# Optimization experiments

Measured on AMD Instinct MI355X. Metric: run time of the kernel, lower is better.

## Reference

```python
import jax, jax.numpy as jnp
import numpy as np

MAX_DEG = 10
MIN_DEG = 0
N_FEAT = 128
NB_FILTER = 128
BATCH = 128
DEG_COUNT = 30000                      # atoms per degree bucket (static)
N_ATOMS = (MAX_DEG + 1) * DEG_COUNT    # 330000, atoms sorted by degree (deg0 first)
NB_AFFINE = 3 * MAX_DEG + (2 - MIN_DEG)  # 32
EPS = 1e-5


def setup_inputs() -> dict:
    key = jax.random.key(0)
    ks = jax.random.split(key, 16)
    atoms = jax.random.normal(ks[0], (N_ATOMS, N_FEAT), dtype=jnp.float32)
    membership = jax.random.randint(ks[1], (N_ATOMS,), 0, BATCH)
    # deg_slice[d] = [start, count] for degree d (atoms sorted by degree)
    deg_slice = jnp.stack([jnp.arange(MAX_DEG + 1) * DEG_COUNT,
                           jnp.full((MAX_DEG + 1,), DEG_COUNT)], axis=1)
    inp = {"atoms": atoms, "deg_slice": deg_slice, "membership": membership}
    for d in range(1, MAX_DEG + 1):
        inp[f"adj{d}"] = jax.random.randint(ks[1 + d], (DEG_COUNT, d), 0, N_ATOMS)
    glorot = (2.0 / (N_FEAT + NB_FILTER)) ** 0.5
    inp["W"] = jax.random.normal(ks[12], (NB_AFFINE, N_FEAT, NB_FILTER), dtype=jnp.float32) * glorot
    inp["b"] = jnp.zeros((NB_AFFINE, NB_FILTER), dtype=jnp.float32)
    inp["gamma"] = jnp.ones((NB_FILTER,), dtype=jnp.float32)
    inp["beta"] = jnp.zeros((NB_FILTER,), dtype=jnp.float32)
    return inp


def _self_slice(atoms, deg):
    return jax.lax.dynamic_slice_in_dim(atoms, deg * DEG_COUNT, DEG_COUNT, axis=0)


def _norm(x, gamma, beta):
    m = jnp.mean(x, axis=-1, keepdims=True)
    std = jnp.sqrt(jnp.var(x, axis=-1, keepdims=True) + EPS)
    return gamma * ((x - m) / (std + EPS)) + beta


def _forward(atoms, W, b, gamma, beta, membership, adjs):
    # W consumption order matches the TF iterator: for deg=1..max_deg -> (rel, self),
    # then deg0 self at index 2*MAX_DEG, then gather affines deg1..max_deg, deg0 last.
    rel_outs = [None] * (MAX_DEG + 1)
    gather_outs = [None] * (MAX_DEG + 1)
    for d in range(1, MAX_DEG + 1):
        neigh = jnp.sum(atoms[adjs[d - 1]], axis=1)          # (COUNT, F) gather+sum
        self_a = _self_slice(atoms, d)                        # (COUNT, F)
        i_rel, i_self = 2 * (d - 1), 2 * d - 1
        rel_outs[d] = (neigh @ W[i_rel] + b[i_rel]) + (self_a @ W[i_self] + b[i_self])
        i_g = 2 * MAX_DEG + d
        gather_outs[d] = self_a @ W[i_g] + b[i_g]
    self0 = _self_slice(atoms, 0)
    rel_outs[0] = self0 @ W[2 * MAX_DEG] + b[2 * MAX_DEG]
    gather_outs[0] = self0 @ W[NB_AFFINE - 1] + b[NB_AFFINE - 1]

    activated = jnp.concatenate(rel_outs, axis=0)             # (N_ATOMS, NB_FILTER)
    gathered = jnp.concatenate(gather_outs, axis=0)           # (N_ATOMS, NB_FILTER)
    # graph_gather: per-molecule sum (dynamic_partition + reduce_sum)
    atom_gather = jax.ops.segment_sum(gathered, membership, num_segments=BATCH)

    xn = _norm(activated, gamma, beta)                        # per-row "BN" as in source
    yn = _norm(atom_gather, gamma, beta)
    # gather_node: per-molecule max of normalized atom features
    g = jax.ops.segment_max(xn, membership, num_segments=BATCH)
    return xn, yn, g


def reference(atoms, deg_slice, membership, adj1, adj2, adj3, adj4, adj5,
              adj6, adj7, adj8, adj9, adj10, W, b, gamma, beta):
    adjs = (adj1, adj2, adj3, adj4, adj5, adj6, adj7, adj8, adj9, adj10)
    return _forward(atoms, W, b, gamma, beta, membership, adjs)
```

## Files before the change

kernel.cpp:

```cpp
#include <hip/hip_runtime.h>
#include <stdint.h>

#define MAX_DEG   10
#define DEG_COUNT 30000
#define N_ATOMS   330000
#define NF        128
#define BATCH     128
#define SORT_BLOCKS 256

typedef __attribute__((ext_vector_type(8))) short bf16x8;
typedef __attribute__((ext_vector_type(4))) float f32x4;

__device__ __forceinline__ float bf2f(unsigned short h) {
  union { unsigned u; float f; } v; v.u = ((unsigned)h) << 16; return v.f;
}
__device__ __forceinline__ unsigned short f2bf(float f) {
  union { float f; unsigned u; } v; v.f = f;
  unsigned u = v.u;
  unsigned r = (u + 0x7fffu + ((u >> 16) & 1u)) >> 16;
  return (unsigned short)r;
}

struct AdjPtrs { const int* p[10]; };

#define NEG_INF_BITS 0xFF800000

__global__ __launch_bounds__(256) void k_cast(const float4* __restrict__ src,
                                              ushort4* __restrict__ dst) {
  size_t i = (size_t)blockIdx.x * 256 + threadIdx.x;
  float4 v = src[i];
  ushort4 o;
  o.x = f2bf(v.x); o.y = f2bf(v.y); o.z = f2bf(v.z); o.w = f2bf(v.w);
  dst[i] = o;
}

__global__ __launch_bounds__(256) void k_build_b(const float* __restrict__ W,
                                                 unsigned short* __restrict__ BcatT) {
  int idx = blockIdx.x * 256 + threadIdx.x;
  if (idx >= 11 * 128 * 256) return;
  int d = idx >> 15;
  int rem = idx & 32767;
  int n = rem >> 8;
  int k = rem & 255;
  float v;
  if (k < 128) {
    v = (d >= 1) ? W[(2 * (d - 1)) * 16384 + k * 128 + n] : 0.f;
  } else {
    int ks = k - 128;
    int wi = (d >= 1) ? (2 * d - 1) : 20;
    v = W[wi * 16384 + ks * 128 + n];
  }
  BcatT[idx] = f2bf(v);
}

__global__ __launch_bounds__(256) void k_build_bias(const float* __restrict__ b,
                                                    float* __restrict__ biascat) {
  int idx = blockIdx.x * 256 + threadIdx.x;
  if (idx >= 11 * 128) return;
  int d = idx >> 7, n = idx & 127;
  float f = (d >= 1) ? (b[(2 * (d - 1)) * 128 + n] + b[(2 * d - 1) * 128 + n])
                     : b[20 * 128 + n];
  biascat[idx] = f;
}

template<int D>
__device__ __forceinline__ void nsum_phase0(const unsigned* __restrict__ atomsU,
                                            const int* __restrict__ abase,
                                            unsigned* __restrict__ NS,
                                            int rowTile, int wave, int lane) {
  for (int it = 0; it < 8; ++it) {
    int iloc = wave * 16 + it * 2;
    int r0 = rowTile * 128 + iloc;
    int sw0 = lane ^ ((iloc & 7) << 2);
    int sw1 = lane ^ (((iloc + 1) & 7) << 2);
    if (r0 < DEG_COUNT - 1) {
      const int* a = abase + (size_t)r0 * D;
      int myIdx = (lane < 2 * D) ? a[lane] : 0;
      unsigned xs[2 * D];
#pragma unroll
      for (int j = 0; j < 2 * D; ++j) {
        int nbr = __shfl(myIdx, j, 64);
        xs[j] = atomsU[(size_t)nbr * 64 + lane];
      }
      float s0a = 0.f, s1a = 0.f, s0b = 0.f, s1b = 0.f;
#pragma unroll
      for (int j = 0; j < D; ++j) {
        s0a += bf2f((unsigned short)(xs[j] & 0xffff));
        s1a += bf2f((unsigned short)(xs[j] >> 16));
      }
#pragma unroll
      for (int j = D; j < 2 * D; ++j) {
        s0b += bf2f((unsigned short)(xs[j] & 0xffff));
        s1b += bf2f((unsigned short)(xs[j] >> 16));
      }
      NS[(size_t)iloc * 64 + sw0]       = (unsigned)f2bf(s0a) | ((unsigned)f2bf(s1a) << 16);
      NS[(size_t)(iloc + 1) * 64 + sw1] = (unsigned)f2bf(s0b) | ((unsigned)f2bf(s1b) << 16);
    } else {
      const int* a = abase + (size_t)(DEG_COUNT - 1) * D;
      int myIdx = (lane < D) ? a[lane] : 0;
      unsigned xs[D];
#pragma unroll
      for (int j = 0; j < D; ++j) {
        int nbr = __shfl(myIdx, j, 64);
        xs[j] = atomsU[(size_t)nbr * 64 + lane];
      }
      float s0 = 0.f, s1 = 0.f;
#pragma unroll
      for (int j = 0; j < D; ++j) {
        s0 += bf2f((unsigned short)(xs[j] & 0xffff));
        s1 += bf2f((unsigned short)(xs[j] >> 16));
      }
      unsigned p = (unsigned)f2bf(s0) | ((unsigned)f2bf(s1) << 16);
      NS[(size_t)iloc * 64 + sw0] = p;
      NS[(size_t)(iloc + 1) * 64 + sw1] = p;
    }
  }
}

__global__ __launch_bounds__(512, 4) void k_gemm(
    const unsigned short* __restrict__ atomsBf,
    AdjPtrs adj,
    const unsigned short* __restrict__ BcatT,
    const float* __restrict__ biascat,
    const float* __restrict__ gamma,
    const float* __restrict__ beta,
    float* __restrict__ out0)
{
  const int d = blockIdx.y;
  const int rowTile = blockIdx.x;
  const int tid = threadIdx.x;
  const int lane = tid & 63;
  const int wave = tid >> 6;
  const int m16 = lane & 15;
  const int g = lane >> 4;

  __shared__ unsigned short Bs[128 * 256];
  unsigned* NS = (unsigned*)Bs;

  const unsigned short* Bd = BcatT + d * 32768;
  const unsigned* atomsU = (const unsigned*)atomsBf;

  const int rowBase = rowTile * 128 + wave * 16;
  bf16x8 af[8];
  {
    int rbL = rowBase + m16; if (rbL > DEG_COUNT - 1) rbL = DEG_COUNT - 1;
    size_t gr = (size_t)d * DEG_COUNT + rbL;
#pragma unroll
    for (int ks = 4; ks < 8; ++ks)
      af[ks] = *(const bf16x8*)(atomsBf + gr * 128 + (ks - 4) * 32 + g * 8);
  }

  if (d > 0) {
    const int* abase = adj.p[d - 1];
    switch (d) {
      case 1:  nsum_phase0<1>(atomsU, abase, NS, rowTile, wave, lane); break;
      case 2:  nsum_phase0<2>(atomsU, abase, NS, rowTile, wave, lane); break;
      case 3:  nsum_phase0<3>(atomsU, abase, NS, rowTile, wave, lane); break;
      case 4:  nsum_phase0<4>(atomsU, abase, NS, rowTile, wave, lane); break;
      case 5:  nsum_phase0<5>(atomsU, abase, NS, rowTile, wave, lane); break;
      case 6:  nsum_phase0<6>(atomsU, abase, NS, rowTile, wave, lane); break;
      case 7:  nsum_phase0<7>(atomsU, abase, NS, rowTile, wave, lane); break;
      case 8:  nsum_phase0<8>(atomsU, abase, NS, rowTile, wave, lane); break;
      case 9:  nsum_phase0<9>(atomsU, abase, NS, rowTile, wave, lane); break;
      default: nsum_phase0<10>(atomsU, abase, NS, rowTile, wave, lane); break;
    }
    __syncthreads();
    const char* nsb = (const char*)NS;
    const int rowb = (wave * 16 + m16) * 256;
    const int sw = (m16 & 7) << 4;
#pragma unroll
    for (int ks = 0; ks < 4; ++ks)
      af[ks] = *(const bf16x8*)(nsb + ((rowb + ks * 64 + g * 16) ^ sw));
    __syncthreads();
  } else {
    bf16x8 z = {0, 0, 0, 0, 0, 0, 0, 0};
#pragma unroll
    for (int ks = 0; ks < 4; ++ks) af[ks] = z;
  }

#pragma unroll
  for (int it = 0; it < 8; ++it) {
    int flat = it * 512 + tid;
    int row = flat >> 5;
    int c = flat & 31;
    uint4 v = *(const uint4*)(Bd + row * 256 + c * 8);
    int kb = (c * 16) ^ ((row & 7) << 4);
    *(uint4*)((char*)Bs + row * 512 + kb) = v;
  }

  __syncthreads();

  const int ldsMask = (m16 & 7) << 4;

  f32x4 acc[8];
#pragma unroll
  for (int ct = 0; ct < 8; ++ct) acc[ct] = (f32x4){0.f, 0.f, 0.f, 0.f};

#pragma unroll
  for (int ct = 0; ct < 8; ++ct) {
    const char* bbase = (const char*)Bs + (ct * 16 + m16) * 512;
    bf16x8 bf[8];
#pragma unroll
    for (int ks = 0; ks < 8; ++ks)
      bf[ks] = *(const bf16x8*)(bbase + ((ks * 64 + g * 16) ^ ldsMask));
#pragma unroll
    for (int ks = 0; ks < 8; ++ks)
      acc[ct] = __builtin_amdgcn_mfma_f32_16x16x32_bf16(af[ks], bf[ks], acc[ct], 0, 0, 0);
  }

  float bias_[8], gam[8], bet[8];
#pragma unroll
  for (int ct = 0; ct < 8; ++ct) {
    bias_[ct] = biascat[d * 128 + ct * 16 + m16];
    gam[ct] = gamma[ct * 16 + m16];
    bet[ct] = beta[ct * 16 + m16];
  }

#pragma unroll
  for (int ct = 0; ct < 8; ++ct)
#pragma unroll
    for (int r = 0; r < 4; ++r) acc[ct][r] += bias_[ct];

  float s[4], qq[4];
#pragma unroll
  for (int r = 0; r < 4; ++r) {
    s[r] = 0.f; qq[r] = 0.f;
#pragma unroll
    for (int ct = 0; ct < 8; ++ct) {
      float v = acc[ct][r];
      s[r] += v; qq[r] += v * v;
    }
  }
#pragma unroll
  for (int off = 8; off >= 1; off >>= 1) {
#pragma unroll
    for (int r = 0; r < 4; ++r) {
      s[r]  += __shfl_xor(s[r],  off, 64);
      qq[r] += __shfl_xor(qq[r], off, 64);
    }
  }

#pragma unroll
  for (int r = 0; r < 4; ++r) {
    int rb = rowBase + g * 4 + r;
    float mean = s[r] * (1.0f / 128.0f);
    float var  = qq[r] * (1.0f / 128.0f) - mean * mean;
    float inv  = 1.0f / (sqrtf(var + 1e-5f) + 1e-5f);
    if (rb < DEG_COUNT) {
      size_t grow = (size_t)d * DEG_COUNT + rb;
#pragma unroll
      for (int ct = 0; ct < 8; ++ct)
        out0[grow * 128 + ct * 16 + m16] = gam[ct] * ((acc[ct][r] - mean) * inv) + bet[ct];
    }
  }
}

__global__ __launch_bounds__(256) void k_hist2(const int* __restrict__ membership,
                                               int* __restrict__ blockHist) {
  __shared__ int bins[BATCH];
  int tid = threadIdx.x;
  if (tid < BATCH) bins[tid] = 0;
  __syncthreads();
  const int chunk = (N_ATOMS + SORT_BLOCKS - 1) / SORT_BLOCKS;
  int lo = blockIdx.x * chunk, hi = min(lo + chunk, N_ATOMS);
  for (int i = lo + tid; i < hi; i += 256)
    atomicAdd(&bins[membership[i]], 1);
  __syncthreads();
  if (tid < BATCH) blockHist[blockIdx.x * BATCH + tid] = bins[tid];
}

__global__ __launch_bounds__(128) void k_scan2(const int* __restrict__ blockHist,
                                               int* __restrict__ off,
                                               int* __restrict__ base,
                                               int* __restrict__ hist) {
  int m = threadIdx.x;
  int tot = 0;
  for (int b = 0; b < SORT_BLOCKS; ++b) tot += blockHist[b * BATCH + m];
  hist[m] = tot;
  __shared__ int t[BATCH];
  t[m] = tot;
  __syncthreads();
  int acc = 0;
  for (int i = 0; i < m; ++i) acc += t[i];
  base[m] = acc;
  int run = acc;
  for (int b = 0; b < SORT_BLOCKS; ++b) {
    off[b * BATCH + m] = run;
    run += blockHist[b * BATCH + m];
  }
}

__global__ __launch_bounds__(256) void k_scatter2(const int* __restrict__ membership,
                                                  const int* __restrict__ off,
                                                  int* __restrict__ perm) {
  __shared__ int bins[BATCH];
  int tid = threadIdx.x;
  if (tid < BATCH) bins[tid] = off[blockIdx.x * BATCH + tid];
  __syncthreads();
  const int chunk = (N_ATOMS + SORT_BLOCKS - 1) / SORT_BLOCKS;
  int lo = blockIdx.x * chunk, hi = min(lo + chunk, N_ATOMS);
  for (int i = lo + tid; i < hi; i += 256) {
    int m = membership[i];
    int pos = atomicAdd(&bins[m], 1);
    perm[pos] = i;
  }
}

__global__ __launch_bounds__(512) void k_msum(
    const unsigned* __restrict__ atomsU,
    const int* __restrict__ perm,
    const int* __restrict__ base,
    const int* __restrict__ hist,
    float* __restrict__ Spart,
    int* __restrict__ cntPart)
{
  const int m = blockIdx.x >> 2;
  const int s = blockIdx.x & 3;
  const int b0 = base[m], cnt = hist[m];
  const int lo = b0 + (cnt * s) / 4;
  const int hi = b0 + (cnt * (s + 1)) / 4;
  const int wave = threadIdx.x >> 6, lane = threadIdx.x & 63;

  __shared__ float S[8][11][128];
  __shared__ int C[8][11];
  for (int e = lane; e < 11 * 128; e += 64) S[wave][e >> 7][e & 127] = 0.f;
  if (lane < 11) C[wave][lane] = 0;
  __syncthreads();

  for (int i = lo + wave; i < hi; i += 8) {
    int r = perm[i];
    int d = r / DEG_COUNT;
    unsigned x = atomsU[(size_t)r * 64 + lane];
    S[wave][d][lane]      += bf2f((unsigned short)(x & 0xffff));
    S[wave][d][64 + lane] += bf2f((unsigned short)(x >> 16));
    if (lane == 0) C[wave][d]++;
  }
  __syncthreads();

  for (int e = threadIdx.x; e < 11 * 128; e += 512) {
    int d = e >> 7, p = e & 127;
    float t = 0.f;
#pragma unroll
    for (int w = 0; w < 8; ++w) t += S[w][d][p];
    int col = (p < 64) ? (2 * p) : (2 * (p - 64) + 1);
    Spart[(((size_t)s * 128 + m) * 11 + d) * 128 + col] = t;
  }
  if (threadIdx.x < 11) {
    int t = 0;
#pragma unroll
    for (int w = 0; w < 8; ++w) t += C[w][threadIdx.x];
    cntPart[((size_t)s * 128 + m) * 11 + threadIdx.x] = t;
  }
}

__global__ __launch_bounds__(128) void k_yn(
    const float* __restrict__ Spart,
    const int* __restrict__ cntPart,
    const float* __restrict__ W,
    const float* __restrict__ b,
    const float* __restrict__ gamma,
    const float* __restrict__ beta,
    float* __restrict__ out1)
{
  int m = blockIdx.x;
  int j = threadIdx.x;
  __shared__ float Sm[11][128];
  __shared__ float cw[11];
  for (int e = j; e < 11 * 128; e += 128) {
    int d = e >> 7, c = e & 127;
    float t = 0.f;
#pragma unroll
    for (int sl = 0; sl < 4; ++sl)
      t += Spart[(((size_t)sl * 128 + m) * 11 + d) * 128 + c];
    Sm[d][c] = t;
  }
  if (j < 11) {
    int t = 0;
#pragma unroll
    for (int sl = 0; sl < 4; ++sl) t += cntPart[((size_t)sl * 128 + m) * 11 + j];
    cw[j] = (float)t;
  }
  __syncthreads();

  float acc = 0.f;
  for (int d = 0; d < 11; ++d) {
    int wi = (d >= 1) ? (20 + d) : 31;
    const float* Wd = W + wi * 16384;
    float a0 = 0.f, a1 = 0.f, a2 = 0.f, a3 = 0.f;
    for (int k = 0; k < 128; k += 4) {
      a0 += Sm[d][k]     * Wd[k * 128 + j];
      a1 += Sm[d][k + 1] * Wd[(k + 1) * 128 + j];
      a2 += Sm[d][k + 2] * Wd[(k + 2) * 128 + j];
      a3 += Sm[d][k + 3] * Wd[(k + 3) * 128 + j];
    }
    acc += (a0 + a1) + (a2 + a3);
    acc += cw[d] * b[wi * 128 + j];
  }

  float ws_ = acc, wq = acc * acc;
#pragma unroll
  for (int off = 32; off >= 1; off >>= 1) {
    ws_ += __shfl_xor(ws_, off, 64);
    wq  += __shfl_xor(wq, off, 64);
  }
  __shared__ float red[4];
  int wave = j >> 6, lane = j & 63;
  if (lane == 0) { red[wave * 2] = ws_; red[wave * 2 + 1] = wq; }
  __syncthreads();
  float Ssum = red[0] + red[2], Q = red[1] + red[3];
  float mean = Ssum * (1.f / 128.f);
  float var = Q * (1.f / 128.f) - mean * mean;
  float inv = 1.f / (sqrtf(var + 1e-5f) + 1e-5f);
  out1[m * 128 + j] = gamma[j] * ((acc - mean) * inv) + beta[j];
}

__global__ __launch_bounds__(512) void k_reduce(
    const float2* __restrict__ xnV,
    const int* __restrict__ perm,
    const int* __restrict__ base,
    const int* __restrict__ hist,
    float2* __restrict__ pmax4)
{
  const int m = blockIdx.x >> 2;
  const int s = blockIdx.x & 3;
  const int b0 = base[m], cnt = hist[m];
  const int lo = b0 + (cnt * s) / 4;
  const int hi = b0 + (cnt * (s + 1)) / 4;
  const int wave = threadIdx.x >> 6, lane = threadIdx.x & 63;

  const float NEG_INF = __int_as_float((int)NEG_INF_BITS);
  float mx0 = NEG_INF, mx1 = NEG_INF;

#pragma unroll 4
  for (int i = lo + wave; i < hi; i += 8) {
    int r = perm[i];
    float2 x = xnV[(size_t)r * 64 + lane];
    mx0 = fmaxf(mx0, x.x);
    mx1 = fmaxf(mx1, x.y);
  }

  __shared__ float2 maxT[8][64];
  maxT[wave][lane] = make_float2(mx0, mx1);
  __syncthreads();

  if (threadIdx.x < 64) {
    int l = threadIdx.x;
    float2 mm = maxT[0][l];
#pragma unroll
    for (int w = 1; w < 8; ++w) {
      float2 b = maxT[w][l]; mm.x = fmaxf(mm.x, b.x); mm.y = fmaxf(mm.y, b.y);
    }
    pmax4[(s * 128 + m) * 64 + l] = mm;
  }
}

__global__ __launch_bounds__(128) void k_final(
    const float* __restrict__ pmax4,
    float* __restrict__ out2)
{
  int m = blockIdx.x;
  int j = threadIdx.x;
  float g = __int_as_float((int)NEG_INF_BITS);
#pragma unroll
  for (int sl = 0; sl < 4; ++sl)
    g = fmaxf(g, pmax4[(sl * 128 + m) * 128 + j]);
  out2[m * 128 + j] = g;
}

extern "C" void kernel_launch(void* const* d_in, const int* in_sizes, int n_in,
                              void* d_out, int out_size, void* d_ws, size_t ws_size,
                              hipStream_t stream) {
  const float* atoms = (const float*)d_in[0];
  const int* membership = (const int*)d_in[2];
  AdjPtrs adj;
  for (int i = 0; i < 10; ++i) adj.p[i] = (const int*)d_in[3 + i];
  const float* W     = (const float*)d_in[13];
  const float* b     = (const float*)d_in[14];
  const float* gamma = (const float*)d_in[15];
  const float* beta  = (const float*)d_in[16];

  char* ws = (char*)d_ws;
  size_t off = 0;
  unsigned short* atomsBf = (unsigned short*)(ws + off); off += (size_t)N_ATOMS * 128 * 2;
  unsigned short* BcatT   = (unsigned short*)(ws + off); off += (size_t)11 * 128 * 256 * 2;
  float* biascat          = (float*)(ws + off);          off += (size_t)11 * 128 * 4;
  int* perm               = (int*)(ws + off);            off += (size_t)N_ATOMS * 4;
  int* hist               = (int*)(ws + off);            off += 512;
  int* base_              = (int*)(ws + off);            off += 512;
  int* blockHist          = (int*)(ws + off);            off += (size_t)SORT_BLOCKS * BATCH * 4;
  int* offTab             = (int*)(ws + off);            off += (size_t)SORT_BLOCKS * BATCH * 4;
  float* Spart            = (float*)(ws + off);          off += (size_t)4 * 128 * 11 * 128 * 4;
  int* cntPart            = (int*)(ws + off);            off += (size_t)4 * 128 * 11 * 4;
  float* pmax4            = (float*)(ws + off);          off += (size_t)4 * 128 * 128 * 4;

  float* out0 = (float*)d_out;
  float* out1 = out0 + (size_t)N_ATOMS * 128;
  float* out2 = out1 + 16384;

  hipLaunchKernelGGL(k_cast, dim3(N_ATOMS * 128 / 4 / 256), dim3(256), 0, stream,
                     (const float4*)atoms, (ushort4*)atomsBf);
  hipLaunchKernelGGL(k_build_b, dim3((11 * 128 * 256 + 255) / 256), dim3(256), 0, stream, W, BcatT);
  hipLaunchKernelGGL(k_build_bias, dim3((11 * 128 + 255) / 256), dim3(256), 0, stream, b, biascat);
  hipLaunchKernelGGL(k_hist2, dim3(SORT_BLOCKS), dim3(256), 0, stream, membership, blockHist);
  hipLaunchKernelGGL(k_scan2, dim3(1), dim3(128), 0, stream, blockHist, offTab, base_, hist);
  hipLaunchKernelGGL(k_scatter2, dim3(SORT_BLOCKS), dim3(256), 0, stream, membership, offTab, perm);
  hipLaunchKernelGGL(k_msum, dim3(512), dim3(512), 0, stream,
                     (const unsigned*)atomsBf, perm, base_, hist, Spart, cntPart);
  hipLaunchKernelGGL(k_gemm, dim3(236, 11), dim3(512), 0, stream,
                     atomsBf, adj, BcatT, biascat, gamma, beta, out0);
  hipLaunchKernelGGL(k_reduce, dim3(512), dim3(512), 0, stream,
                     (const float2*)out0, perm, base_, hist, (float2*)pmax4);
  hipLaunchKernelGGL(k_yn, dim3(128), dim3(128), 0, stream,
                     Spart, cntPart, W, b, gamma, beta, out1);
  hipLaunchKernelGGL(k_final, dim3(128), dim3(128), 0, stream, pmax4, out2);
}
```

Baseline: 554.5 us.

## Fuse molecule sum and max reductions into one pass, add nontemporal memory ops

Merges the per-molecule bf16 atom sum (k_msum) and the per-molecule max over normalized outputs (k_reduce) into a single kernel that walks the permutation once and reads both arrays per row. It also folds k_final into k_yn, which removes two launches. The cast kernel's loads, the GEMM epilogue's output stores and the fused reduction's loads are now nontemporal, to limit cache pollution on streaming traffic. The trade-off is that the molecule-sum work now runs after the GEMM instead of before it, and the fused loop carries two gather streams per iteration. The `#pragma unroll 4` that k_reduce had on this loop is dropped.

```diff
diff --git a/kernel.cpp b/kernel.cpp
--- a/kernel.cpp
+++ b/kernel.cpp
@@ -10,6 +10,7 @@
 
 typedef __attribute__((ext_vector_type(8))) short bf16x8;
 typedef __attribute__((ext_vector_type(4))) float f32x4;
+typedef __attribute__((ext_vector_type(2))) float f32x2;
 
 __device__ __forceinline__ float bf2f(unsigned short h) {
   union { unsigned u; float f; } v; v.u = ((unsigned)h) << 16; return v.f;
@@ -25,12 +26,12 @@
 
 #define NEG_INF_BITS 0xFF800000
 
-__global__ __launch_bounds__(256) void k_cast(const float4* __restrict__ src,
+__global__ __launch_bounds__(256) void k_cast(const f32x4* __restrict__ src,
                                               ushort4* __restrict__ dst) {
   size_t i = (size_t)blockIdx.x * 256 + threadIdx.x;
-  float4 v = src[i];
+  f32x4 v = __builtin_nontemporal_load(src + i);
   ushort4 o;
-  o.x = f2bf(v.x); o.y = f2bf(v.y); o.z = f2bf(v.z); o.w = f2bf(v.w);
+  o.x = f2bf(v[0]); o.y = f2bf(v[1]); o.z = f2bf(v[2]); o.w = f2bf(v[3]);
   dst[i] = o;
 }
 
@@ -249,8 +250,10 @@
     if (rb < DEG_COUNT) {
       size_t grow = (size_t)d * DEG_COUNT + rb;
 #pragma unroll
-      for (int ct = 0; ct < 8; ++ct)
-        out0[grow * 128 + ct * 16 + m16] = gam[ct] * ((acc[ct][r] - mean) * inv) + bet[ct];
+      for (int ct = 0; ct < 8; ++ct) {
+        float v = gam[ct] * ((acc[ct][r] - mean) * inv) + bet[ct];
+        __builtin_nontemporal_store(v, out0 + grow * 128 + ct * 16 + m16);
+      }
     }
   }
 }
@@ -306,13 +309,15 @@
   }
 }
 
-__global__ __launch_bounds__(512) void k_msum(
+__global__ __launch_bounds__(512) void k_mreduce(
+    const f32x2* __restrict__ xnV,
     const unsigned* __restrict__ atomsU,
     const int* __restrict__ perm,
     const int* __restrict__ base,
     const int* __restrict__ hist,
     float* __restrict__ Spart,
-    int* __restrict__ cntPart)
+    int* __restrict__ cntPart,
+    float2* __restrict__ pmax4)
 {
   const int m = blockIdx.x >> 2;
   const int s = blockIdx.x & 3;
@@ -323,20 +328,37 @@
 
   __shared__ float S[8][11][128];
   __shared__ int C[8][11];
+  __shared__ float2 maxT[8][64];
   for (int e = lane; e < 11 * 128; e += 64) S[wave][e >> 7][e & 127] = 0.f;
   if (lane < 11) C[wave][lane] = 0;
   __syncthreads();
+
+  const float NEG_INF = __int_as_float((int)NEG_INF_BITS);
+  float mx0 = NEG_INF, mx1 = NEG_INF;
 
   for (int i = lo + wave; i < hi; i += 8) {
     int r = perm[i];
     int d = r / DEG_COUNT;
-    unsigned x = atomsU[(size_t)r * 64 + lane];
-    S[wave][d][lane]      += bf2f((unsigned short)(x & 0xffff));
-    S[wave][d][64 + lane] += bf2f((unsigned short)(x >> 16));
+    f32x2 x = __builtin_nontemporal_load(xnV + (size_t)r * 64 + lane);
+    unsigned a = __builtin_nontemporal_load(atomsU + (size_t)r * 64 + lane);
+    mx0 = fmaxf(mx0, x[0]);
+    mx1 = fmaxf(mx1, x[1]);
+    S[wave][d][lane]      += bf2f((unsigned short)(a & 0xffff));
+    S[wave][d][64 + lane] += bf2f((unsigned short)(a >> 16));
     if (lane == 0) C[wave][d]++;
   }
-  __syncthreads();
-
+  maxT[wave][lane] = make_float2(mx0, mx1);
+  __syncthreads();
+
+  if (threadIdx.x < 64) {
+    int l = threadIdx.x;
+    float2 mm = maxT[0][l];
+#pragma unroll
+    for (int w = 1; w < 8; ++w) {
+      float2 b = maxT[w][l]; mm.x = fmaxf(mm.x, b.x); mm.y = fmaxf(mm.y, b.y);
+    }
+    pmax4[(s * 128 + m) * 64 + l] = mm;
+  }
   for (int e = threadIdx.x; e < 11 * 128; e += 512) {
     int d = e >> 7, p = e & 127;
     float t = 0.f;
@@ -353,17 +375,26 @@
   }
 }
 
-__global__ __launch_bounds__(128) void k_yn(
+__global__ __launch_bounds__(128) void k_ynfinal(
     const float* __restrict__ Spart,
     const int* __restrict__ cntPart,
     const float* __restrict__ W,
     const float* __restrict__ b,
     const float* __restrict__ gamma,
     const float* __restrict__ beta,
-    float* __restrict__ out1)
+    const float* __restrict__ pmax4,
+    float* __restrict__ out1,
+    float* __restrict__ out2)
 {
   int m = blockIdx.x;
   int j = threadIdx.x;
+
+  float g = __int_as_float((int)NEG_INF_BITS);
+#pragma unroll
+  for (int sl = 0; sl < 4; ++sl)
+    g = fmaxf(g, pmax4[(sl * 128 + m) * 128 + j]);
+  out2[m * 128 + j] = g;
+
   __shared__ float Sm[11][128];
   __shared__ float cw[11];
   for (int e = j; e < 11 * 128; e += 128) {
@@ -412,59 +443,6 @@
   float var = Q * (1.f / 128.f) - mean * mean;
   float inv = 1.f / (sqrtf(var + 1e-5f) + 1e-5f);
   out1[m * 128 + j] = gamma[j] * ((acc - mean) * inv) + beta[j];
-}
-
-__global__ __launch_bounds__(512) void k_reduce(
-    const float2* __restrict__ xnV,
-    const int* __restrict__ perm,
-    const int* __restrict__ base,
-    const int* __restrict__ hist,
-    float2* __restrict__ pmax4)
-{
-  const int m = blockIdx.x >> 2;
-  const int s = blockIdx.x & 3;
-  const int b0 = base[m], cnt = hist[m];
-  const int lo = b0 + (cnt * s) / 4;
-  const int hi = b0 + (cnt * (s + 1)) / 4;
-  const int wave = threadIdx.x >> 6, lane = threadIdx.x & 63;
-
-  const float NEG_INF = __int_as_float((int)NEG_INF_BITS);
-  float mx0 = NEG_INF, mx1 = NEG_INF;
-
-#pragma unroll 4
-  for (int i = lo + wave; i < hi; i += 8) {
-    int r = perm[i];
-    float2 x = xnV[(size_t)r * 64 + lane];
-    mx0 = fmaxf(mx0, x.x);
-    mx1 = fmaxf(mx1, x.y);
-  }
-
-  __shared__ float2 maxT[8][64];
-  maxT[wave][lane] = make_float2(mx0, mx1);
-  __syncthreads();
-
-  if (threadIdx.x < 64) {
-    int l = threadIdx.x;
-    float2 mm = maxT[0][l];
-#pragma unroll
-    for (int w = 1; w < 8; ++w) {
-      float2 b = maxT[w][l]; mm.x = fmaxf(mm.x, b.x); mm.y = fmaxf(mm.y, b.y);
-    }
-    pmax4[(s * 128 + m) * 64 + l] = mm;
-  }
-}
-
-__global__ __launch_bounds__(128) void k_final(
-    const float* __restrict__ pmax4,
-    float* __restrict__ out2)
-{
-  int m = blockIdx.x;
-  int j = threadIdx.x;
-  float g = __int_as_float((int)NEG_INF_BITS);
-#pragma unroll
-  for (int sl = 0; sl < 4; ++sl)
-    g = fmaxf(g, pmax4[(sl * 128 + m) * 128 + j]);
-  out2[m * 128 + j] = g;
 }
 
 extern "C" void kernel_launch(void* const* d_in, const int* in_sizes, int n_in,
@@ -498,19 +476,17 @@
   float* out2 = out1 + 16384;
 
   hipLaunchKernelGGL(k_cast, dim3(N_ATOMS * 128 / 4 / 256), dim3(256), 0, stream,
-                     (const float4*)atoms, (ushort4*)atomsBf);
+                     (const f32x4*)atoms, (ushort4*)atomsBf);
   hipLaunchKernelGGL(k_build_b, dim3((11 * 128 * 256 + 255) / 256), dim3(256), 0, stream, W, BcatT);
   hipLaunchKernelGGL(k_build_bias, dim3((11 * 128 + 255) / 256), dim3(256), 0, stream, b, biascat);
   hipLaunchKernelGGL(k_hist2, dim3(SORT_BLOCKS), dim3(256), 0, stream, membership, blockHist);
   hipLaunchKernelGGL(k_scan2, dim3(1), dim3(128), 0, stream, blockHist, offTab, base_, hist);
   hipLaunchKernelGGL(k_scatter2, dim3(SORT_BLOCKS), dim3(256), 0, stream, membership, offTab, perm);
-  hipLaunchKernelGGL(k_msum, dim3(512), dim3(512), 0, stream,
-                     (const unsigned*)atomsBf, perm, base_, hist, Spart, cntPart);
   hipLaunchKernelGGL(k_gemm, dim3(236, 11), dim3(512), 0, stream,
                      atomsBf, adj, BcatT, biascat, gamma, beta, out0);
-  hipLaunchKernelGGL(k_reduce, dim3(512), dim3(512), 0, stream,
-                     (const float2*)out0, perm, base_, hist, (float2*)pmax4);
-  hipLaunchKernelGGL(k_yn, dim3(128), dim3(128), 0, stream,
-                     Spart, cntPart, W, b, gamma, beta, out1);
-  hipLaunchKernelGGL(k_final, dim3(128), dim3(128), 0, stream, pmax4, out2);
-}
+  hipLaunchKernelGGL(k_mreduce, dim3(512), dim3(512), 0, stream,
+                     (const f32x2*)out0, (const unsigned*)atomsBf, perm, base_, hist,
+                     Spart, cntPart, (float2*)pmax4);
+  hipLaunchKernelGGL(k_ynfinal, dim3(128), dim3(128), 0, stream,
+                     Spart, cntPart, W, b, gamma, beta, pmax4, out1, out2);
+}
```

After: 552.0 us. No clear change (-0.4%).
